# Optimization experiments

Measured on AMD Instinct MI355X. Metric: run time of the kernel, lower is better.

The kernel has to match this reference:

```python
import jax, jax.numpy as jnp
import numpy as np

EPS = 1e-5
D_MODEL, N_HEADS, D_FF, SEQ, BATCH, THETA = 1024, 16, 4096, 2048, 4, 10000.0


def rmsnorm(x, g):
    rms = jnp.sqrt(jnp.mean(jnp.square(x), axis=-1, keepdims=True) + EPS)
    return (x / rms) * g


def rope(x, pos, theta):
    # x: [B, H, S, Dh]; pos: [S]
    dh = x.shape[-1]
    inv_freq = theta ** (-jnp.arange(0, dh, 2, dtype=x.dtype) / dh)  # [Dh/2]
    ang = pos.astype(x.dtype)[:, None] * inv_freq                    # [S, Dh/2]
    cos, sin = jnp.cos(ang), jnp.sin(ang)
    x1, x2 = x[..., ::2], x[..., 1::2]
    r1 = x1 * cos - x2 * sin
    r2 = x1 * sin + x2 * cos
    return jnp.stack([r1, r2], axis=-1).reshape(x.shape)


def setup_inputs() -> dict:
    key = jax.random.key(0)
    ks = jax.random.split(key, 10)
    s = 0.02
    return {
        "x": jax.random.normal(ks[0], (BATCH, SEQ, D_MODEL), jnp.float32),
        "token_positions": jnp.arange(SEQ, dtype=jnp.int64 if jax.config.x64_enabled else jnp.int32),
        "g1": jnp.ones((D_MODEL,), jnp.float32),
        "g2": jnp.ones((D_MODEL,), jnp.float32),
        "wq": jax.random.normal(ks[1], (D_MODEL, D_MODEL), jnp.float32) * s,
        "wk": jax.random.normal(ks[2], (D_MODEL, D_MODEL), jnp.float32) * s,
        "wv": jax.random.normal(ks[3], (D_MODEL, D_MODEL), jnp.float32) * s,
        "wo": jax.random.normal(ks[4], (D_MODEL, D_MODEL), jnp.float32) * s,
        "w1": jax.random.normal(ks[5], (D_MODEL, D_FF), jnp.float32) * s,
        "w2": jax.random.normal(ks[6], (D_FF, D_MODEL), jnp.float32) * s,
        "w3": jax.random.normal(ks[7], (D_MODEL, D_FF), jnp.float32) * s,
    }


def reference(x, token_positions, g1, g2, wq, wk, wv, wo, w1, w2, w3):
    B, S, D = x.shape
    H = N_HEADS
    Dh = D // H

    # --- RMSNorm 1 + causal RoPE self-attention ---
    h = rmsnorm(x, g1)
    q = (h @ wq).reshape(B, S, H, Dh).transpose(0, 2, 1, 3)  # [B,H,S,Dh]
    k = (h @ wk).reshape(B, S, H, Dh).transpose(0, 2, 1, 3)
    v = (h @ wv).reshape(B, S, H, Dh).transpose(0, 2, 1, 3)
    q = rope(q, token_positions, THETA)
    k = rope(k, token_positions, THETA)

    scores = jnp.einsum("bhqd,bhkd->bhqk", q, k) / jnp.sqrt(jnp.asarray(Dh, x.dtype))
    causal = jnp.tril(jnp.ones((S, S), bool))
    scores = jnp.where(causal, scores, jnp.asarray(-jnp.inf, x.dtype))
    attn = jax.nn.softmax(scores, axis=-1)
    ctx = jnp.einsum("bhqk,bhkd->bhqd", attn, v)             # [B,H,S,Dh]
    ctx = ctx.transpose(0, 2, 1, 3).reshape(B, S, D)
    attn_out = ctx @ wo

    y = x + attn_out  # residual

    # --- RMSNorm 2 + SwiGLU ---
    h2 = rmsnorm(y, g2)
    gate = jax.nn.silu(h2 @ w1) * (h2 @ w3)
    ff = gate @ w2

    return y + ff
```

## Files before the change

### kernel.cpp

```cpp
#include <hip/hip_runtime.h>
#include <hip/hip_bf16.h>
#include <cstdint>
#include <cstddef>

typedef __bf16 bf16_t;
typedef __bf16 bf16x8 __attribute__((ext_vector_type(8)));
typedef __bf16 bf16x4 __attribute__((ext_vector_type(4)));
typedef float  f32x4  __attribute__((ext_vector_type(4)));

#define D_MODEL 1024
#define SEQ     2048
#define NHEADS  16
#define DHEAD   64
#define DFF     4096

__device__ __forceinline__ void async_ld16(void* lds, const void* g) {
    __builtin_amdgcn_global_load_lds(
        (__attribute__((address_space(1))) void*)(void*)(g),
        (__attribute__((address_space(3))) void*)(lds), 16, 0, 0);
}

__device__ __forceinline__ void xcd_swizzle(int& bx, int& by) {
    const int gy = gridDim.y;
    const int i = blockIdx.x + gridDim.x * blockIdx.y;
    if ((gy & 7) == 0) {
        const int cy = gy >> 3;
        const int xcd = i & 7, j = i >> 3;
        bx = j / cy;
        by = xcd * cy + (j % cy);
    } else { bx = blockIdx.x; by = blockIdx.y; }
}

__global__ __launch_bounds__(256)
void transpose_cast_kernel(const float* __restrict__ src, bf16_t* __restrict__ dst,
                           int K, int N, int gstride, int goff)
{
    __shared__ float tile[32][33];
    const int bn = blockIdx.x * 32, bk = blockIdx.y * 32;
    const int tx = threadIdx.x & 31, ty = threadIdx.x >> 5;
#pragma unroll
    for (int i = 0; i < 32; i += 8)
        tile[ty + i][tx] = src[(size_t)(bk + ty + i) * N + bn + tx];
    __syncthreads();
#pragma unroll
    for (int i = 0; i < 32; i += 8) {
        const int n = bn + ty + i, kk = bk + tx;
        const int row = (n >> 4) * gstride + (n & 15) + goff;
        dst[(size_t)row * K + kk] = (bf16_t)tile[tx][ty + i];
    }
}

__global__ __launch_bounds__(256)
void transpose_v_kernel(const bf16_t* __restrict__ v, bf16_t* __restrict__ vt)
{
    __shared__ bf16_t T[64 * 66];
    const int bh = blockIdx.y, s0 = blockIdx.x * 64;
    const int tid = threadIdx.x;
    const size_t vb = (size_t)bh * SEQ * DHEAD;
#pragma unroll
    for (int h = 0; h < 2; ++h) {
        const int s = h * 32 + (tid >> 3), dc = (tid & 7) * 8;
        const bf16x8 vv = *(const bf16x8*)(v + vb + (size_t)(s0 + s) * DHEAD + dc);
#pragma unroll
        for (int j = 0; j < 8; ++j) T[(dc + j) * 66 + s] = vv[j];
    }
    __syncthreads();
    const size_t tb = (size_t)bh * DHEAD * SEQ;
    const uint32_t* Tw = (const uint32_t*)T;
#pragma unroll
    for (int h = 0; h < 2; ++h) {
        const int dh = h * 32 + (tid >> 3), kc = (tid & 7) * 8;
        uint4 o;
        o.x = Tw[dh * 33 + kc / 2 + 0];
        o.y = Tw[dh * 33 + kc / 2 + 1];
        o.z = Tw[dh * 33 + kc / 2 + 2];
        o.w = Tw[dh * 33 + kc / 2 + 3];
        *(uint4*)(vt + tb + (size_t)((s0 + kc) >> 3) * 512 + dh * 8) = o;
    }
}

__global__ __launch_bounds__(256)
void rmsnorm_kernel(const float* __restrict__ x, const float* __restrict__ gw,
                    bf16_t* __restrict__ out)
{
    const int row = blockIdx.x, tid = threadIdx.x;
    const float4 v = ((const float4*)(x + (size_t)row * D_MODEL))[tid];
    float ss = v.x*v.x + v.y*v.y + v.z*v.z + v.w*v.w;
#pragma unroll
    for (int d = 1; d < 64; d <<= 1) ss += __shfl_xor(ss, d);
    __shared__ float red[4];
    if ((tid & 63) == 0) red[tid >> 6] = ss;
    __syncthreads();
    const float tot = red[0] + red[1] + red[2] + red[3];
    const float sc = rsqrtf(tot * (1.f / D_MODEL) + 1e-5f);
    const float4 gv = ((const float4*)gw)[tid];
    bf16x4 o;
    o[0] = (bf16_t)(v.x * sc * gv.x);
    o[1] = (bf16_t)(v.y * sc * gv.y);
    o[2] = (bf16_t)(v.z * sc * gv.z);
    o[3] = (bf16_t)(v.w * sc * gv.w);
    ((bf16x4*)(out + (size_t)row * D_MODEL))[tid] = o;
}

template <int MODE>
__global__ __launch_bounds__(512, 2)
void gemm256_kernel(const bf16_t* __restrict__ A, const bf16_t* __restrict__ Bt,
                    int M, int N, int K,
                    bf16_t* __restrict__ qo, bf16_t* __restrict__ ko, bf16_t* __restrict__ vo,
                    bf16_t* __restrict__ gate)
{
    __shared__ bf16x8 lds[8192];
    const int tid  = threadIdx.x;
    const int wave = tid >> 6;
    const int lane = tid & 63;
    const int r = lane & 15, g = lane >> 4;
    const int wm = wave >> 2;
    const int wn = wave & 3;
    const int r3 = (r >> 3) & 1;
    const int gx = g ^ (((r >> 2) & 1) << 1);
    const int cx0 = r3 * 4 + gx;
    const int cx1 = cx0 ^ 4;

    int bx, by;
    xcd_swizzle(bx, by);
    const int row0 = by * 256;
    const int col0 = bx * 256;

    const f32x4 fzero = {0.f, 0.f, 0.f, 0.f};
    f32x4 acc[8][4];
#pragma unroll
    for (int i = 0; i < 8; ++i)
#pragma unroll
        for (int j = 0; j < 4; ++j) acc[i][j] = fzero;

    const int kcx = ((tid & 7) ^ (((tid >> 5) & 1) << 1) ^ (((tid >> 6) & 1) << 2)) * 8;
    const bf16_t* aSrc = A  + (size_t)(row0 + (tid >> 3)) * K + kcx;
    const bf16_t* bSrc = Bt + (size_t)(col0 + (tid >> 3)) * K + kcx;

    const int aRB = wm * 1024 + r * 8;
    const int bRB = 2048 + (wn >> 1) * 1024 + ((wn & 1) * 64 + r) * 8;

#define STA(nb, ktn, h_, j_) \
    async_ld16(&lds[(nb) + (h_) * 1024 + (j_) * 512 + tid], \
               aSrc + (size_t)((h_) * 128 + (j_) * 64) * K + (ktn))
#define STB(nb, ktn, h_, j_) \
    async_ld16(&lds[(nb) + 2048 + (h_) * 1024 + (j_) * 512 + tid], \
               bSrc + (size_t)((h_) * 128 + (j_) * 64) * K + (ktn))

    STB(0, 0, 0, 0); STB(0, 0, 0, 1); STB(0, 0, 1, 0); STB(0, 0, 1, 1);
    STA(0, 0, 0, 0); STA(0, 0, 1, 0);
    STA(0, 0, 0, 1); STA(0, 0, 1, 1);
    asm volatile("s_waitcnt vmcnt(2)" ::: "memory");
    __builtin_amdgcn_s_barrier();

    bf16x8 aF[8], bF[8];

    const int NT = K >> 6;
    for (int t = 0; t < NT; ++t) {
        const int AB  = (t & 1) << 12;
        const int nb  = AB ^ 4096;
        const int ktn = (t + 1) << 6;
        const bool pf = (t + 1) < NT;

#pragma unroll
        for (int q = 0; q < 4; ++q) {
            aF[q * 2 + 0] = lds[AB + aRB + q * 128 + cx0];
            aF[q * 2 + 1] = lds[AB + aRB + q * 128 + cx1];
        }
#pragma unroll
        for (int n = 0; n < 2; ++n) {
            bF[n * 2 + 0] = lds[AB + bRB + n * 128 + cx0];
            bF[n * 2 + 1] = lds[AB + bRB + n * 128 + cx1];
        }
        if (pf) { STB(nb, ktn, 0, 0); STB(nb, ktn, 0, 1); }
        __builtin_amdgcn_s_barrier();
        asm volatile("s_waitcnt lgkmcnt(0)" ::: "memory");
        __builtin_amdgcn_sched_barrier(0);
        __builtin_amdgcn_s_setprio(1);
#pragma unroll
        for (int q = 0; q < 4; ++q)
#pragma unroll
            for (int n = 0; n < 2; ++n)
#pragma unroll
                for (int ks = 0; ks < 2; ++ks)
                    acc[q][n] = __builtin_amdgcn_mfma_f32_16x16x32_bf16(
                        aF[q * 2 + ks], bF[n * 2 + ks], acc[q][n], 0, 0, 0);
        __builtin_amdgcn_s_setprio(0);
        __builtin_amdgcn_s_barrier();

#pragma unroll
        for (int n = 0; n < 2; ++n) {
            bF[4 + n * 2 + 0] = lds[AB + bRB + (32 + n * 16) * 8 + cx0];
            bF[4 + n * 2 + 1] = lds[AB + bRB + (32 + n * 16) * 8 + cx1];
        }
        if (pf) { STB(nb, ktn, 1, 0); STB(nb, ktn, 1, 1); }
        __builtin_amdgcn_s_barrier();
        asm volatile("s_waitcnt lgkmcnt(0)" ::: "memory");
        __builtin_amdgcn_sched_barrier(0);
        __builtin_amdgcn_s_setprio(1);
#pragma unroll
        for (int q = 0; q < 4; ++q)
#pragma unroll
            for (int n = 0; n < 2; ++n)
#pragma unroll
                for (int ks = 0; ks < 2; ++ks)
                    acc[q][2 + n] = __builtin_amdgcn_mfma_f32_16x16x32_bf16(
                        aF[q * 2 + ks], bF[4 + n * 2 + ks], acc[q][2 + n], 0, 0, 0);
        __builtin_amdgcn_s_setprio(0);
        if (pf) asm volatile("s_waitcnt vmcnt(4)" ::: "memory");
        else    asm volatile("s_waitcnt vmcnt(0)" ::: "memory");
        __builtin_amdgcn_s_barrier();

#pragma unroll
        for (int q = 0; q < 4; ++q) {
            aF[q * 2 + 0] = lds[AB + aRB + (64 + q * 16) * 8 + cx0];
            aF[q * 2 + 1] = lds[AB + aRB + (64 + q * 16) * 8 + cx1];
        }
        if (pf) { STA(nb, ktn, 0, 0); STA(nb, ktn, 1, 0); }
        __builtin_amdgcn_s_barrier();
        asm volatile("s_waitcnt lgkmcnt(0)" ::: "memory");
        __builtin_amdgcn_sched_barrier(0);
        __builtin_amdgcn_s_setprio(1);
#pragma unroll
        for (int q = 0; q < 4; ++q)
#pragma unroll
            for (int n = 0; n < 2; ++n)
#pragma unroll
                for (int ks = 0; ks < 2; ++ks)
                    acc[4 + q][2 + n] = __builtin_amdgcn_mfma_f32_16x16x32_bf16(
                        aF[q * 2 + ks], bF[4 + n * 2 + ks], acc[4 + q][2 + n], 0, 0, 0);
        __builtin_amdgcn_s_setprio(0);
        __builtin_amdgcn_s_barrier();

        if (pf) { STA(nb, ktn, 0, 1); STA(nb, ktn, 1, 1); }
        __builtin_amdgcn_s_barrier();
        __builtin_amdgcn_s_setprio(1);
#pragma unroll
        for (int q = 0; q < 4; ++q)
#pragma unroll
            for (int n = 0; n < 2; ++n)
#pragma unroll
                for (int ks = 0; ks < 2; ++ks)
                    acc[4 + q][n] = __builtin_amdgcn_mfma_f32_16x16x32_bf16(
                        aF[q * 2 + ks], bF[n * 2 + ks], acc[4 + q][n], 0, 0, 0);
        __builtin_amdgcn_s_setprio(0);
        if (pf) asm volatile("s_waitcnt vmcnt(2)" ::: "memory");
        __builtin_amdgcn_s_barrier();
    }
#undef STA
#undef STB

    const int mbase = row0 + wm * 128 + g * 4;
    const int nbase = col0 + wn * 64 + r;

    if constexpr (MODE == 2) {
#pragma unroll
        for (int np = 0; np < 2; ++np) {
            const int gc = (col0 >> 1) + wn * 32 + np * 16 + r;
#pragma unroll
            for (int mt = 0; mt < 8; ++mt) {
#pragma unroll
                for (int e = 0; e < 4; ++e) {
                    const float v1 = acc[mt][2 * np][e];
                    const float v3 = acc[mt][2 * np + 1][e];
                    const float sv = v1 * __builtin_amdgcn_rcpf(1.f + __expf(-v1));
                    const int grow = mbase + mt * 16 + e;
                    gate[(size_t)grow * DFF + gc] = (bf16_t)(sv * v3);
                }
            }
        }
    } else {
#pragma unroll
        for (int nt = 0; nt < 4; ++nt) {
            const int gcol = nbase + nt * 16;
            const int mat  = gcol >> 10;
            const int d    = gcol & 1023;
            const int head = d >> 6;
            const int dh   = d & 63;
            const float invf = __expf((float)(dh & ~1) * -0.14391157f);
            const size_t hb = (size_t)head * SEQ * DHEAD + dh;
#pragma unroll
            for (int mt = 0; mt < 8; ++mt) {
#pragma unroll
                for (int e = 0; e < 4; ++e) {
                    const float val = acc[mt][nt][e];
                    const float partner = __shfl_xor(val, 1);
                    const int grow = mbase + mt * 16 + e;
                    const int b = grow >> 11;
                    const int s = grow & 2047;
                    const size_t dst = (size_t)b * NHEADS * SEQ * DHEAD + hb + (size_t)s * DHEAD;
                    if (mat == 2) {
                        vo[dst] = (bf16_t)val;
                    } else {
                        float sn, cs;
                        __sincosf((float)s * invf, &sn, &cs);
                        const float rv = (dh & 1) ? (partner * sn + val * cs)
                                                  : (val * cs - partner * sn);
                        if (mat == 0) qo[dst] = (bf16_t)(rv * 0.125f);
                        else          ko[dst] = (bf16_t)rv;
                    }
                }
            }
        }
    }
}

template <int MODE>
__global__ __launch_bounds__(256, 3)
void gemm128_kernel(const bf16_t* __restrict__ A, const bf16_t* __restrict__ Bt,
                    int M, int N, int K, const float* res, float* outf)
{
    __shared__ bf16x8 Al[1024];
    __shared__ bf16x8 Bl[1024];
    const int tid  = threadIdx.x;
    const int wave = tid >> 6;
    const int lane = tid & 63;
    const int r    = lane & 15;
    const int g    = lane >> 4;
    const int wm   = wave >> 1;
    const int wn   = wave & 1;
    const int r3 = (r >> 3) & 1;
    const int gx = g ^ (((r >> 2) & 1) << 1);
    const int cx0 = r3 * 4 + gx;
    const int cx1 = cx0 ^ 4;

    int bx, by;
    xcd_swizzle(bx, by);
    const int row0 = by * 128;
    const int col0 = bx * 128;

    const f32x4 fzero = {0.f, 0.f, 0.f, 0.f};
    f32x4 acc[4][4];
#pragma unroll
    for (int i = 0; i < 4; ++i)
#pragma unroll
        for (int j = 0; j < 4; ++j) acc[i][j] = fzero;

    const int kcx = ((tid & 7) ^ (((tid >> 5) & 1) << 1) ^ (((tid >> 6) & 1) << 2)) * 8;
    const bf16_t* a0 = A  + (size_t)(row0 + (tid >> 3)) * K + kcx;
    const bf16_t* b0 = Bt + (size_t)(col0 + (tid >> 3)) * K + kcx;

    for (int kt = 0; kt < K; kt += 64) {
#pragma unroll
        for (int j = 0; j < 4; ++j)
            async_ld16(&Al[j * 256 + tid], a0 + kt + (size_t)(j * 32) * K);
#pragma unroll
        for (int j = 0; j < 4; ++j)
            async_ld16(&Bl[j * 256 + tid], b0 + kt + (size_t)(j * 32) * K);
        __syncthreads();
#pragma unroll
        for (int s = 0; s < 2; ++s) {
            const int cx = s ? cx1 : cx0;
            bf16x8 af[4], bfr[4];
#pragma unroll
            for (int mt = 0; mt < 4; ++mt) af[mt]  = Al[(wm * 64 + mt * 16 + r) * 8 + cx];
#pragma unroll
            for (int nt = 0; nt < 4; ++nt) bfr[nt] = Bl[(wn * 64 + nt * 16 + r) * 8 + cx];
#pragma unroll
            for (int mt = 0; mt < 4; ++mt)
#pragma unroll
                for (int nt = 0; nt < 4; ++nt)
                    acc[mt][nt] = __builtin_amdgcn_mfma_f32_16x16x32_bf16(
                        af[mt], bfr[nt], acc[mt][nt], 0, 0, 0);
        }
        __syncthreads();
    }

    const int mbase = row0 + wm * 64 + g * 4;
    const int nbase = col0 + wn * 64 + r;
#pragma unroll
    for (int mt = 0; mt < 4; ++mt) {
#pragma unroll
        for (int nt = 0; nt < 4; ++nt) {
#pragma unroll
            for (int e = 0; e < 4; ++e) {
                const int grow = mbase + mt * 16 + e;
                const int gcol = nbase + nt * 16;
                const size_t idx = (size_t)grow * D_MODEL + gcol;
                outf[idx] = res[idx] + acc[mt][nt][e];
            }
        }
    }
}

__global__ __launch_bounds__(256, 4)
void attn_kernel(const bf16_t* __restrict__ qg, const bf16_t* __restrict__ kg,
                 const bf16_t* __restrict__ vT, bf16_t* __restrict__ ctx)
{
    __shared__ bf16x8 lds[2048];
    const int qblk = (gridDim.x - 1) - blockIdx.x;
    const int bh   = blockIdx.y;
    const int tid  = threadIdx.x;
    const int wave = tid >> 6;
    const int lane = tid & 63;
    const int r = lane & 15, g = lane >> 4;
    const size_t base = (size_t)bh * SEQ * DHEAD;
    const int qw = qblk * 128 + wave * 32;

    bf16x8 qf[2][2];
#pragma unroll
    for (int rt = 0; rt < 2; ++rt)
#pragma unroll
        for (int kh = 0; kh < 2; ++kh)
            qf[rt][kh] = *(const bf16x8*)(qg + base + (size_t)(qw + rt*16 + r) * DHEAD + kh*32 + g*8);

    const f32x4 fzero = {0.f, 0.f, 0.f, 0.f};
    f32x4 O[2][4];
    float mi[2][4], li[2][4];
#pragma unroll
    for (int rt = 0; rt < 2; ++rt)
#pragma unroll
        for (int e = 0; e < 4; ++e) { mi[rt][e] = -1e30f; li[rt][e] = 0.f; }
#pragma unroll
    for (int rt = 0; rt < 2; ++rt)
#pragma unroll
        for (int d = 0; d < 4; ++d) O[rt][d] = fzero;

    bf16_t* const Pb = (bf16_t*)&lds[1024 + wave * 256];
    const int pcx = ((r >> 2) & 3) << 1;

    const int NKB = 2 * qblk + 2;
    for (int kb = 0; kb < NKB; ++kb) {
        const int k0 = kb * 64;
        {
            const bf16_t* kp = kg + base + (size_t)(k0 + lane) * DHEAD + wave * 8;
            async_ld16(&lds[tid], kp);
            async_ld16(&lds[256 + tid], kp + 32);
        }
        {
            const bf16_t* vp = vT + base + (size_t)k0 * DHEAD + tid * 8;
            async_ld16(&lds[512 + tid], vp);
            async_ld16(&lds[768 + tid], vp + 2048);
        }
        __syncthreads();

        if (k0 <= qw + 31) {
            f32x4 sc[2][4];
            __builtin_amdgcn_s_setprio(1);
#pragma unroll
            for (int ct = 0; ct < 4; ++ct) {
                const bf16x8 kf0 = lds[g * 64 + ct * 16 + r];
                const bf16x8 kf1 = lds[(4 + g) * 64 + ct * 16 + r];
                sc[0][ct] = __builtin_amdgcn_mfma_f32_16x16x32_bf16(qf[0][0], kf0, fzero, 0, 0, 0);
                sc[0][ct] = __builtin_amdgcn_mfma_f32_16x16x32_bf16(qf[0][1], kf1, sc[0][ct], 0, 0, 0);
                sc[1][ct] = __builtin_amdgcn_mfma_f32_16x16x32_bf16(qf[1][0], kf0, fzero, 0, 0, 0);
                sc[1][ct] = __builtin_amdgcn_mfma_f32_16x16x32_bf16(qf[1][1], kf1, sc[1][ct], 0, 0, 0);
            }
            __builtin_amdgcn_s_setprio(0);
            if (k0 + 63 > qw) {
#pragma unroll
                for (int rt = 0; rt < 2; ++rt)
#pragma unroll
                    for (int ct = 0; ct < 4; ++ct)
#pragma unroll
                        for (int e = 0; e < 4; ++e)
                            if (k0 + ct * 16 + r > qw + rt * 16 + g * 4 + e)
                                sc[rt][ct][e] = -1e30f;
            }
#pragma unroll
            for (int rt = 0; rt < 2; ++rt) {
#pragma unroll
                for (int e = 0; e < 4; ++e) {
                    float mx = fmaxf(fmaxf(sc[rt][0][e], sc[rt][1][e]),
                                     fmaxf(sc[rt][2][e], sc[rt][3][e]));
#pragma unroll
                    for (int d = 1; d < 16; d <<= 1) mx = fmaxf(mx, __shfl_xor(mx, d));
                    const float mnew  = fmaxf(mi[rt][e], mx);
                    const float alpha = __expf(mi[rt][e] - mnew);
                    mi[rt][e] = mnew;
                    float pv[4], rs = 0.f;
#pragma unroll
                    for (int ct = 0; ct < 4; ++ct) { pv[ct] = __expf(sc[rt][ct][e] - mnew); rs += pv[ct]; }
#pragma unroll
                    for (int d = 1; d < 16; d <<= 1) rs += __shfl_xor(rs, d);
                    li[rt][e] = li[rt][e] * alpha + rs;
#pragma unroll
                    for (int dht = 0; dht < 4; ++dht) O[rt][dht][e] *= alpha;
                    const int qlocal = rt * 16 + g * 4 + e;
#pragma unroll
                    for (int ct = 0; ct < 4; ++ct)
                        Pb[qlocal * 64 + ((ct * 16 + r) ^ (g << 4))] = (bf16_t)pv[ct];
                }
            }
            __builtin_amdgcn_s_setprio(1);
#pragma unroll
            for (int kt = 0; kt < 2; ++kt) {
                const int cix = (kt * 4 + g) ^ pcx;
                const bf16x8 pf0 = lds[1024 + wave * 256 + r * 8 + cix];
                const bf16x8 pf1 = lds[1024 + wave * 256 + 128 + r * 8 + cix];
#pragma unroll
                for (int dht = 0; dht < 4; ++dht) {
                    const bf16x8 vf = lds[512 + (kt * 4 + g) * 64 + dht * 16 + r];
                    O[0][dht] = __builtin_amdgcn_mfma_f32_16x16x32_bf16(pf0, vf, O[0][dht], 0, 0, 0);
                    O[1][dht] = __builtin_amdgcn_mfma_f32_16x16x32_bf16(pf1, vf, O[1][dht], 0, 0, 0);
                }
            }
            __builtin_amdgcn_s_setprio(0);
        }
        __syncthreads();
    }

    const int b = bh >> 4, head = bh & 15;
#pragma unroll
    for (int rt = 0; rt < 2; ++rt) {
#pragma unroll
        for (int e = 0; e < 4; ++e) {
            const float inv = __builtin_amdgcn_rcpf(li[rt][e]);
            const int s = qw + rt * 16 + g * 4 + e;
            bf16_t* op = ctx + ((size_t)(b * SEQ + s)) * D_MODEL + head * DHEAD + r;
#pragma unroll
            for (int dht = 0; dht < 4; ++dht)
                op[dht * 16] = (bf16_t)(O[rt][dht][e] * inv);
        }
    }
}

extern "C" void kernel_launch(void* const* d_in, const int* in_sizes, int n_in,
                              void* d_out, int out_size, void* d_ws, size_t ws_size,
                              hipStream_t stream)
{
    (void)in_sizes; (void)n_in; (void)out_size; (void)ws_size;
    const float* x  = (const float*)d_in[0];
    const float* g1 = (const float*)d_in[2];
    const float* g2 = (const float*)d_in[3];
    const float* wq = (const float*)d_in[4];
    const float* wk = (const float*)d_in[5];
    const float* wv = (const float*)d_in[6];
    const float* wo = (const float*)d_in[7];
    const float* w1 = (const float*)d_in[8];
    const float* w2 = (const float*)d_in[9];
    const float* w3 = (const float*)d_in[10];
    float* out = (float*)d_out;
    char* ws = (char*)d_ws;
    const size_t MB = 1ull << 20;
    bf16_t* wqkvT = (bf16_t*)(ws + 0);
    bf16_t* woT   = (bf16_t*)(ws + 6  * MB);
    bf16_t* w13T  = (bf16_t*)(ws + 8  * MB);
    bf16_t* w2T   = (bf16_t*)(ws + 24 * MB);
    bf16_t* hbuf  = (bf16_t*)(ws + 32 * MB);
    bf16_t* qbuf  = (bf16_t*)(ws + 48 * MB);
    bf16_t* kbuf  = (bf16_t*)(ws + 64 * MB);
    bf16_t* vbuf  = (bf16_t*)(ws + 80 * MB);
    bf16_t* ctx   = (bf16_t*)(ws + 96 * MB);
    bf16_t* gate  = (bf16_t*)(ws + 48 * MB);
    bf16_t* vTb   = hbuf;

    dim3 blk(256);
    dim3 blk5(512);
    transpose_cast_kernel<<<dim3(32, 32),  blk, 0, stream>>>(wq, wqkvT,             1024, 1024, 16, 0);
    transpose_cast_kernel<<<dim3(32, 32),  blk, 0, stream>>>(wk, wqkvT + 1024*1024, 1024, 1024, 16, 0);
    transpose_cast_kernel<<<dim3(32, 32),  blk, 0, stream>>>(wv, wqkvT + 2048*1024, 1024, 1024, 16, 0);
    transpose_cast_kernel<<<dim3(32, 32),  blk, 0, stream>>>(wo, woT,               1024, 1024, 16, 0);
    transpose_cast_kernel<<<dim3(128, 32), blk, 0, stream>>>(w1, w13T,              1024, 4096, 32, 0);
    transpose_cast_kernel<<<dim3(128, 32), blk, 0, stream>>>(w3, w13T,              1024, 4096, 32, 16);
    transpose_cast_kernel<<<dim3(32, 128), blk, 0, stream>>>(w2, w2T,               4096, 1024, 16, 0);

    rmsnorm_kernel<<<dim3(8192), blk, 0, stream>>>(x, g1, hbuf);

    gemm256_kernel<0><<<dim3(12, 32), blk5, 0, stream>>>(hbuf, wqkvT, 8192, 3072, 1024,
        qbuf, kbuf, vbuf, nullptr);

    transpose_v_kernel<<<dim3(32, 64), blk, 0, stream>>>(vbuf, vTb);

    attn_kernel<<<dim3(16, 64), blk, 0, stream>>>(qbuf, kbuf, vTb, ctx);

    gemm128_kernel<1><<<dim3(8, 64), blk, 0, stream>>>(ctx, woT, 8192, 1024, 1024, x, out);

    rmsnorm_kernel<<<dim3(8192), blk, 0, stream>>>(out, g2, hbuf);

    gemm256_kernel<2><<<dim3(32, 32), blk5, 0, stream>>>(hbuf, w13T, 8192, 8192, 1024,
        nullptr, nullptr, nullptr, gate);

    gemm128_kernel<3><<<dim3(8, 64), blk, 0, stream>>>(gate, w2T, 8192, 1024, 4096, out, out);
}
```

Measured before the change: 699.2 us.

## Double-buffer K/V tiles and add lazy softmax rescale with MFMA row sums

Attention now double-buffers K/V tiles in LDS, prefetching the next block asynchronously while computing the current one, and waits with partial vmcnt. It also skips the online-softmax rescale when the running max grows by no more than a threshold across the wave, and computes row sums of P with an extra MFMA against a ones vector instead of shuffle reductions. This is meant to hide global load latency and cut VALU/shuffle work. In exchange LDS use grows, launch bounds drop occupancy from 4 to 3, and the lazy rescale allows exponents up to e^8 in bf16 P.

```diff
diff --git a/kernel.cpp b/kernel.cpp
--- a/kernel.cpp
+++ b/kernel.cpp
@@ -383,11 +383,11 @@
     }
 }
 
-__global__ __launch_bounds__(256, 4)
+__global__ __launch_bounds__(256, 3)
 void attn_kernel(const bf16_t* __restrict__ qg, const bf16_t* __restrict__ kg,
                  const bf16_t* __restrict__ vT, bf16_t* __restrict__ ctx)
 {
-    __shared__ bf16x8 lds[2048];
+    __shared__ bf16x8 lds[3072];
     const int qblk = (gridDim.x - 1) - blockIdx.x;
     const int bh   = blockIdx.y;
     const int tid  = threadIdx.x;
@@ -405,6 +405,10 @@
             qf[rt][kh] = *(const bf16x8*)(qg + base + (size_t)(qw + rt*16 + r) * DHEAD + kh*32 + g*8);
 
     const f32x4 fzero = {0.f, 0.f, 0.f, 0.f};
+    bf16x8 onesf;
+#pragma unroll
+    for (int j = 0; j < 8; ++j) onesf[j] = (bf16_t)1.f;
+
     f32x4 O[2][4];
     float mi[2][4], li[2][4];
 #pragma unroll
@@ -416,31 +420,36 @@
 #pragma unroll
         for (int d = 0; d < 4; ++d) O[rt][d] = fzero;
 
-    bf16_t* const Pb = (bf16_t*)&lds[1024 + wave * 256];
+    bf16_t* const Pb = (bf16_t*)&lds[2048 + wave * 256];
     const int pcx = ((r >> 2) & 3) << 1;
 
+#define STAGEKV(k0_, B_) { \
+        const bf16_t* kp_ = kg + base + (size_t)((k0_) + lane) * DHEAD + wave * 8; \
+        async_ld16(&lds[(B_) * 512 + tid], kp_); \
+        async_ld16(&lds[(B_) * 512 + 256 + tid], kp_ + 32); \
+        const bf16_t* vp_ = vT + base + (size_t)(k0_) * DHEAD + tid * 8; \
+        async_ld16(&lds[1024 + (B_) * 512 + tid], vp_); \
+        async_ld16(&lds[1024 + (B_) * 512 + 256 + tid], vp_ + 2048); }
+
     const int NKB = 2 * qblk + 2;
+    STAGEKV(0, 0);
     for (int kb = 0; kb < NKB; ++kb) {
         const int k0 = kb * 64;
-        {
-            const bf16_t* kp = kg + base + (size_t)(k0 + lane) * DHEAD + wave * 8;
-            async_ld16(&lds[tid], kp);
-            async_ld16(&lds[256 + tid], kp + 32);
-        }
-        {
-            const bf16_t* vp = vT + base + (size_t)k0 * DHEAD + tid * 8;
-            async_ld16(&lds[512 + tid], vp);
-            async_ld16(&lds[768 + tid], vp + 2048);
-        }
+        const bool pf = (kb + 1) < NKB;
+        if (pf) STAGEKV((kb + 1) * 64, (kb + 1) & 1);
+        if (pf) asm volatile("s_waitcnt vmcnt(4)" ::: "memory");
+        else    asm volatile("s_waitcnt vmcnt(0)" ::: "memory");
         __syncthreads();
 
         if (k0 <= qw + 31) {
+            const int KB = (kb & 1) * 512;
+            const int VB = 1024 + (kb & 1) * 512;
             f32x4 sc[2][4];
             __builtin_amdgcn_s_setprio(1);
 #pragma unroll
             for (int ct = 0; ct < 4; ++ct) {
-                const bf16x8 kf0 = lds[g * 64 + ct * 16 + r];
-                const bf16x8 kf1 = lds[(4 + g) * 64 + ct * 16 + r];
+                const bf16x8 kf0 = lds[KB + g * 64 + ct * 16 + r];
+                const bf16x8 kf1 = lds[KB + 256 + g * 64 + ct * 16 + r];
                 sc[0][ct] = __builtin_amdgcn_mfma_f32_16x16x32_bf16(qf[0][0], kf0, fzero, 0, 0, 0);
                 sc[0][ct] = __builtin_amdgcn_mfma_f32_16x16x32_bf16(qf[0][1], kf1, sc[0][ct], 0, 0, 0);
                 sc[1][ct] = __builtin_amdgcn_mfma_f32_16x16x32_bf16(qf[1][0], kf0, fzero, 0, 0, 0);
@@ -457,48 +466,71 @@
                             if (k0 + ct * 16 + r > qw + rt * 16 + g * 4 + e)
                                 sc[rt][ct][e] = -1e30f;
             }
-#pragma unroll
-            for (int rt = 0; rt < 2; ++rt) {
+            float mx[2][4];
+#pragma unroll
+            for (int rt = 0; rt < 2; ++rt)
 #pragma unroll
                 for (int e = 0; e < 4; ++e) {
-                    float mx = fmaxf(fmaxf(sc[rt][0][e], sc[rt][1][e]),
-                                     fmaxf(sc[rt][2][e], sc[rt][3][e]));
-#pragma unroll
-                    for (int d = 1; d < 16; d <<= 1) mx = fmaxf(mx, __shfl_xor(mx, d));
-                    const float mnew  = fmaxf(mi[rt][e], mx);
-                    const float alpha = __expf(mi[rt][e] - mnew);
-                    mi[rt][e] = mnew;
-                    float pv[4], rs = 0.f;
-#pragma unroll
-                    for (int ct = 0; ct < 4; ++ct) { pv[ct] = __expf(sc[rt][ct][e] - mnew); rs += pv[ct]; }
-#pragma unroll
-                    for (int d = 1; d < 16; d <<= 1) rs += __shfl_xor(rs, d);
-                    li[rt][e] = li[rt][e] * alpha + rs;
-#pragma unroll
-                    for (int dht = 0; dht < 4; ++dht) O[rt][dht][e] *= alpha;
+                    float m = fmaxf(fmaxf(sc[rt][0][e], sc[rt][1][e]),
+                                    fmaxf(sc[rt][2][e], sc[rt][3][e]));
+#pragma unroll
+                    for (int d = 1; d < 16; d <<= 1) m = fmaxf(m, __shfl_xor(m, d));
+                    mx[rt][e] = m;
+                }
+            float worst = mx[0][0] - mi[0][0];
+#pragma unroll
+            for (int rt = 0; rt < 2; ++rt)
+#pragma unroll
+                for (int e = 0; e < 4; ++e)
+                    worst = fmaxf(worst, mx[rt][e] - mi[rt][e]);
+            if (!__all(worst <= 8.f)) {
+#pragma unroll
+                for (int rt = 0; rt < 2; ++rt)
+#pragma unroll
+                    for (int e = 0; e < 4; ++e) {
+                        const float mnew  = fmaxf(mi[rt][e], mx[rt][e]);
+                        const float alpha = __expf(mi[rt][e] - mnew);
+                        mi[rt][e] = mnew;
+                        li[rt][e] *= alpha;
+#pragma unroll
+                        for (int dht = 0; dht < 4; ++dht) O[rt][dht][e] *= alpha;
+                    }
+            }
+#pragma unroll
+            for (int rt = 0; rt < 2; ++rt)
+#pragma unroll
+                for (int e = 0; e < 4; ++e) {
                     const int qlocal = rt * 16 + g * 4 + e;
 #pragma unroll
                     for (int ct = 0; ct < 4; ++ct)
-                        Pb[qlocal * 64 + ((ct * 16 + r) ^ (g << 4))] = (bf16_t)pv[ct];
+                        Pb[qlocal * 64 + ((ct * 16 + r) ^ (g << 4))] =
+                            (bf16_t)__expf(sc[rt][ct][e] - mi[rt][e]);
                 }
-            }
+            f32x4 S[2] = {fzero, fzero};
             __builtin_amdgcn_s_setprio(1);
 #pragma unroll
             for (int kt = 0; kt < 2; ++kt) {
                 const int cix = (kt * 4 + g) ^ pcx;
-                const bf16x8 pf0 = lds[1024 + wave * 256 + r * 8 + cix];
-                const bf16x8 pf1 = lds[1024 + wave * 256 + 128 + r * 8 + cix];
+                const bf16x8 pf0 = lds[2048 + wave * 256 + r * 8 + cix];
+                const bf16x8 pf1 = lds[2048 + wave * 256 + 128 + r * 8 + cix];
 #pragma unroll
                 for (int dht = 0; dht < 4; ++dht) {
-                    const bf16x8 vf = lds[512 + (kt * 4 + g) * 64 + dht * 16 + r];
+                    const bf16x8 vf = lds[VB + (kt * 4 + g) * 64 + dht * 16 + r];
                     O[0][dht] = __builtin_amdgcn_mfma_f32_16x16x32_bf16(pf0, vf, O[0][dht], 0, 0, 0);
                     O[1][dht] = __builtin_amdgcn_mfma_f32_16x16x32_bf16(pf1, vf, O[1][dht], 0, 0, 0);
                 }
+                S[0] = __builtin_amdgcn_mfma_f32_16x16x32_bf16(pf0, onesf, S[0], 0, 0, 0);
+                S[1] = __builtin_amdgcn_mfma_f32_16x16x32_bf16(pf1, onesf, S[1], 0, 0, 0);
             }
             __builtin_amdgcn_s_setprio(0);
+#pragma unroll
+            for (int rt = 0; rt < 2; ++rt)
+#pragma unroll
+                for (int e = 0; e < 4; ++e) li[rt][e] += S[rt][e];
         }
         __syncthreads();
     }
+#undef STAGEKV
 
     const int b = bh >> 4, head = bh & 15;
 #pragma unroll
```

Result: faster. 678.5 us (-3.0%).
